# Performance work log

Hardware: AMD Instinct MI355X
Metric: run time of the kernel (lower is better)

The kernel has to match this reference:

```python
import jax, jax.numpy as jnp
import numpy as np

IN_DIM = 8192
OUT_DIM = 4096
NNZ = 1638400
BATCH = 4096


def setup_inputs() -> dict:
    key = jax.random.key(0)
    k_x, k_r, k_c, k_w = jax.random.split(key, 4)
    x = jax.random.normal(k_x, (BATCH, IN_DIM), dtype=jnp.float32)
    row_idx = jax.random.randint(k_r, (NNZ,), 0, IN_DIM, dtype=jnp.int64)
    col_idx = jax.random.randint(k_c, (NNZ,), 0, OUT_DIM, dtype=jnp.int64)
    # xavier_uniform on a [nnz, 1] tensor: bound = sqrt(6 / (nnz + 1))
    bound = float(np.sqrt(6.0 / (NNZ + 1)))
    weights = jax.random.uniform(k_w, (NNZ,), dtype=jnp.float32, minval=-bound, maxval=bound)
    bias = jnp.zeros((OUT_DIM,), dtype=jnp.float32)
    return {"x": x, "row_idx": row_idx, "col_idx": col_idx, "weights": weights, "bias": bias}


def reference(x, row_idx, col_idx, weights, bias):
    # scatter_nd: build dense [IN_DIM, OUT_DIM] weight matrix via scatter-add
    ind1d = row_idx * OUT_DIM + col_idx  # flat indices, duplicates accumulate
    W = jnp.zeros((IN_DIM * OUT_DIM,), dtype=weights.dtype).at[ind1d].add(weights)
    W = W.reshape(IN_DIM, OUT_DIM)
    # dense matmul + bias, matching torch.mm(x, sparse_tensor) + bias
    return x @ W + bias
```

## Files before the change

kernel.cpp:

```cpp
#include <hip/hip_runtime.h>
#include <stdint.h>

#define IN_DIM 8192
#define OUT_DIM 4096
#define NNZ 1638400
#define BATCH 4096

typedef __bf16 bf16x8 __attribute__((ext_vector_type(8)));
typedef float f32x4 __attribute__((ext_vector_type(4)));


__device__ __forceinline__ unsigned short f2bf(float f) {
  union { float f; unsigned int u; } v; v.f = f;
  unsigned int u = v.u;
  unsigned int r = (u + 0x7FFFu + ((u >> 16) & 1u)) >> 16;
  return (unsigned short)r;
}

__device__ __forceinline__ float bf2f(unsigned short b) {
  union { unsigned int u; float f; } v;
  v.u = (unsigned int)b << 16;
  return v.f;
}

__device__ __forceinline__ void async16(const void* g, void* l) {
  __builtin_amdgcn_global_load_lds(
      (const __attribute__((address_space(1))) unsigned int*)g,
      (__attribute__((address_space(3))) unsigned int*)l,
      16, 0, 0);
}

__device__ __forceinline__ void convert_body(int i, const float* __restrict__ src,
                                             unsigned short* __restrict__ dst) {
  const float4* s = (const float4*)src;
  float4 a = s[2 * i];
  float4 b = s[2 * i + 1];
  union { unsigned short us[8]; uint4 v; } o;
  o.us[0] = f2bf(a.x); o.us[1] = f2bf(a.y); o.us[2] = f2bf(a.z); o.us[3] = f2bf(a.w);
  o.us[4] = f2bf(b.x); o.us[5] = f2bf(b.y); o.us[6] = f2bf(b.z); o.us[7] = f2bf(b.w);
  ((uint4*)dst)[i] = o.v;
}


#define PREP_BLOCKS ((IN_DIM * OUT_DIM) / 8 / 256)

__global__ void prep_kernel(uint4* __restrict__ W_zero,
                            const float* __restrict__ x,
                            unsigned short* __restrict__ x_bf16) {
  int i = blockIdx.x * 256 + threadIdx.x;
  W_zero[i] = make_uint4(0, 0, 0, 0);
  convert_body(i, x, x_bf16);
}


__device__ __forceinline__ void scat1(int c, int r, float w,
                                      unsigned int* __restrict__ W) {
  size_t e = (size_t)c * IN_DIM + r;
  unsigned int* p = W + (e >> 1);
  const bool hi = (e & 1);
  unsigned int cur = *p;
  unsigned int assumed;
  do {
    assumed = cur;
    unsigned short h = hi ? (unsigned short)(assumed >> 16)
                          : (unsigned short)(assumed & 0xFFFFu);
    unsigned short nb = f2bf(bf2f(h) + w);
    unsigned int nw = hi ? ((assumed & 0x0000FFFFu) | ((unsigned int)nb << 16))
                         : ((assumed & 0xFFFF0000u) | (unsigned int)nb);
    cur = atomicCAS(p, assumed, nw);
  } while (cur != assumed);
}

#define SCAT_BLOCKS (NNZ / 4 / 256)

__global__ void scatter_kernel(const int4* __restrict__ ri4,
                               const int4* __restrict__ ci4,
                               const float4* __restrict__ w4,
                               unsigned int* __restrict__ W) {
  int i = blockIdx.x * 256 + threadIdx.x;
  int4 r = ri4[i];
  int4 c = ci4[i];
  float4 w = w4[i];
  scat1(c.x, r.x, w.x, W);
  scat1(c.y, r.y, w.y, W);
  scat1(c.z, r.z, w.z, W);
  scat1(c.w, r.w, w.w, W);
}


#define TBM 256
#define TBN 256
#define TBK 64
#define NKT (IN_DIM / TBK)

__global__ __launch_bounds__(512, 2) void gemm_kernel(
    const unsigned short* __restrict__ A,
    const unsigned short* __restrict__ Bt,
    const float* __restrict__ bias,
    float* __restrict__ C) {
  extern __shared__ __align__(16) unsigned short lds[];

  const int tid = threadIdx.x;

  const int bid = blockIdx.x;
  const int xcd = bid & 7;
  const int j = bid >> 3;
  const int m0 = ((xcd & 1) * 8 + (j & 7)) * TBM;
  const int n0 = ((xcd >> 1) * 4 + (j >> 3)) * TBN;

  const int wid = tid >> 6;
  const int lane = tid & 63;
  const int wm = wid >> 2;
  const int wn = wid & 3;
  const int quad = lane >> 4;
  const int lm = lane & 15;
  const int xorv = lm & 7;

  const unsigned short* Ab = A + (size_t)m0 * IN_DIM;
  const unsigned short* Bb = Bt + (size_t)n0 * IN_DIM;

  int soff[4], ldst[4];
#pragma unroll
  for (int c = 0; c < 4; ++c) {
    const int t2 = c * 512 + tid;
    const int srow = t2 >> 3;
    const int sgs = (t2 & 7) ^ (srow & 7);
    soff[c] = srow * IN_DIM + sgs * 8;
    ldst[c] = t2 * 16;
  }

  f32x4 acc[8][4] = {};

#define STAGE(kt_, b_, c_)                                                  \
  do {                                                                      \
    const int k0_ = (kt_)*TBK;                                              \
    char* la_ = (char*)lds + (b_)*65536;                                    \
    async16(Ab + (size_t)soff[c_] + k0_, la_ + ldst[c_]);                   \
    async16(Bb + (size_t)soff[c_] + k0_, la_ + 32768 + ldst[c_]);           \
  } while (0)

#pragma unroll
  for (int c = 0; c < 4; ++c) STAGE(0, 0, c);

  for (int kt = 0; kt < NKT; ++kt) {
    const int buf = kt & 1;
    const int nbuf = buf ^ 1;
    const int ktn = (kt + 1) & (NKT - 1);

    asm volatile("s_waitcnt vmcnt(0)" ::: "memory");
    __builtin_amdgcn_sched_barrier(0);
    __builtin_amdgcn_s_barrier();
    __builtin_amdgcn_sched_barrier(0);

#pragma unroll
    for (int c = 0; c < 4; ++c) STAGE(ktn, nbuf, c);

    const unsigned short* lA = lds + buf * 32768;
    const unsigned short* lB = lA + 16384;

    bf16x8 bfr[4][2];
#pragma unroll
    for (int j2 = 0; j2 < 4; ++j2) {
      const int row = wn * 64 + j2 * 16 + lm;
#pragma unroll
      for (int ss = 0; ss < 2; ++ss) {
        const int p = ((ss << 2) | quad) ^ xorv;
        bfr[j2][ss] = *(const bf16x8*)(lB + row * TBK + p * 8);
      }
    }

#pragma unroll
    for (int q = 0; q < 4; ++q) {
      bf16x8 af[2][2];
#pragma unroll
      for (int i = 0; i < 2; ++i) {
        const int row = wm * 128 + (q * 2 + i) * 16 + lm;
#pragma unroll
        for (int ss = 0; ss < 2; ++ss) {
          const int p = ((ss << 2) | quad) ^ xorv;
          af[i][ss] = *(const bf16x8*)(lA + row * TBK + p * 8);
        }
      }
      __builtin_amdgcn_s_setprio(1);
#pragma unroll
      for (int i = 0; i < 2; ++i)
#pragma unroll
        for (int j2 = 0; j2 < 4; ++j2)
#pragma unroll
          for (int ss = 0; ss < 2; ++ss)
            acc[q * 2 + i][j2] = __builtin_amdgcn_mfma_f32_16x16x32_bf16(
                af[i][ss], bfr[j2][ss], acc[q * 2 + i][j2], 0, 0, 0);
      __builtin_amdgcn_s_setprio(0);
    }
  }
#undef STAGE

  asm volatile("s_waitcnt vmcnt(0)" ::: "memory");

  const int ccol0 = n0 + wn * 64 + lm;
  const int crow0 = m0 + wm * 128;
#pragma unroll
  for (int j2 = 0; j2 < 4; ++j2) {
    const int col = ccol0 + j2 * 16;
    const float bv = bias[col];
#pragma unroll
    for (int i = 0; i < 8; ++i) {
#pragma unroll
      for (int v = 0; v < 4; ++v) {
        const int row = crow0 + i * 16 + quad * 4 + v;
        C[(size_t)row * OUT_DIM + col] = acc[i][j2][v] + bv;
      }
    }
  }
}


extern "C" void kernel_launch(void* const* d_in, const int* in_sizes, int n_in,
                              void* d_out, int out_size, void* d_ws, size_t ws_size,
                              hipStream_t stream) {
  const float* x = (const float*)d_in[0];
  const int* row_idx = (const int*)d_in[1];
  const int* col_idx = (const int*)d_in[2];
  const float* weights = (const float*)d_in[3];
  const float* bias = (const float*)d_in[4];
  float* out = (float*)d_out;

  const size_t W_BF16_BYTES = (size_t)IN_DIM * OUT_DIM * 2;
  unsigned short* W_bf16 = (unsigned short*)d_ws;
  unsigned short* x_bf16 = (unsigned short*)((char*)d_ws + W_BF16_BYTES);

  static bool attr_set = false;
  if (!attr_set) {
    (void)hipFuncSetAttribute((const void*)gemm_kernel,
                              hipFuncAttributeMaxDynamicSharedMemorySize,
                              131072);
    attr_set = true;
  }

  prep_kernel<<<PREP_BLOCKS, 256, 0, stream>>>((uint4*)W_bf16, x, x_bf16);

  scatter_kernel<<<SCAT_BLOCKS, 256, 0, stream>>>(
      (const int4*)row_idx, (const int4*)col_idx, (const float4*)weights,
      (unsigned int*)W_bf16);

  gemm_kernel<<<dim3(256), dim3(512), 131072, stream>>>(x_bf16, W_bf16, bias, out);
}
```

Measured before the change: 506.6 us.

## Software-pipeline LDS fragment reads across K-tiles in the GEMM main loop

Restructures the GEMM K loop, unrolled by two with ping-pong register sets, so the B fragments and first A fragments for the next tile are read from LDS before the last MFMA group of the current tile runs. The global-load wait and barrier move to inside the tile, so LDS read latency at the start of each tile overlaps with MFMA work. The cost is more live registers from the doubled fragment sets, which could cause spills under the 2-blocks-per-CU launch bound. It also adds a second barrier per tile.

```diff
diff --git a/kernel.cpp b/kernel.cpp
--- a/kernel.cpp
+++ b/kernel.cpp
@@ -104,9 +104,9 @@
 
   const int bid = blockIdx.x;
   const int xcd = bid & 7;
-  const int j = bid >> 3;
-  const int m0 = ((xcd & 1) * 8 + (j & 7)) * TBM;
-  const int n0 = ((xcd >> 1) * 4 + (j >> 3)) * TBN;
+  const int jb = bid >> 3;
+  const int m0 = ((xcd & 1) * 8 + (jb & 7)) * TBM;
+  const int n0 = ((xcd >> 1) * 4 + (jb >> 3)) * TBN;
 
   const int wid = tid >> 6;
   const int lane = tid & 63;
@@ -139,60 +139,95 @@
     async16(Bb + (size_t)soff[c_] + k0_, la_ + 32768 + ldst[c_]);           \
   } while (0)
 
+#define RD_AF(lAp_, q_, AFD)                                                \
+  do {                                                                      \
+    _Pragma("unroll") for (int i = 0; i < 2; ++i) {                         \
+      const int row = wm * 128 + ((q_)*2 + i) * 16 + lm;                    \
+      _Pragma("unroll") for (int ss = 0; ss < 2; ++ss) {                    \
+        const int p = ((ss << 2) | quad) ^ xorv;                            \
+        AFD[i][ss] = *(const bf16x8*)((lAp_) + row * TBK + p * 8);          \
+      }                                                                     \
+    }                                                                       \
+  } while (0)
+
+#define RD_BF(lBp_, BFD)                                                    \
+  do {                                                                      \
+    _Pragma("unroll") for (int j2 = 0; j2 < 4; ++j2) {                      \
+      const int row = wn * 64 + j2 * 16 + lm;                               \
+      _Pragma("unroll") for (int ss = 0; ss < 2; ++ss) {                    \
+        const int p = ((ss << 2) | quad) ^ xorv;                            \
+        BFD[j2][ss] = *(const bf16x8*)((lBp_) + row * TBK + p * 8);         \
+      }                                                                     \
+    }                                                                       \
+  } while (0)
+
+#define MFMA_Q(q_, AF, BFR)                                                 \
+  do {                                                                      \
+    __builtin_amdgcn_s_setprio(1);                                          \
+    _Pragma("unroll") for (int i = 0; i < 2; ++i)                           \
+    _Pragma("unroll") for (int j2 = 0; j2 < 4; ++j2)                        \
+    _Pragma("unroll") for (int ss = 0; ss < 2; ++ss)                        \
+      acc[(q_)*2 + i][j2] = __builtin_amdgcn_mfma_f32_16x16x32_bf16(        \
+          AF[i][ss], BFR[j2][ss], acc[(q_)*2 + i][j2], 0, 0, 0);            \
+    __builtin_amdgcn_s_setprio(0);                                          \
+  } while (0)
+
+#define TILE(t_, buf_, BFRC, AFC, BFRN, AFN)                                \
+  do {                                                                      \
+    const int nb_ = (buf_) ^ 1;                                             \
+    const int ktn_ = ((t_) + 1) & (NKT - 1);                                \
+    const unsigned short* lA_ = lds + (buf_)*32768;                         \
+                  \
+    __builtin_amdgcn_sched_barrier(0);                                      \
+    __builtin_amdgcn_s_barrier();                                           \
+    __builtin_amdgcn_sched_barrier(0);                                      \
+    _Pragma("unroll") for (int c = 0; c < 4; ++c) STAGE(ktn_, nb_, c);      \
+                                   \
+    MFMA_Q(0, AFC, BFRC);                                                   \
+    {                                                                       \
+      bf16x8 afx[2][2];                                                     \
+      RD_AF(lA_, 1, afx);                                                   \
+      MFMA_Q(1, afx, BFRC);                                                 \
+    }                                                                       \
+    {                                                                       \
+      bf16x8 afx[2][2];                                                     \
+      RD_AF(lA_, 2, afx);                                                   \
+      MFMA_Q(2, afx, BFRC);                                                 \
+    }                                                                       \
+    {                                                                       \
+      bf16x8 afx[2][2];                                                     \
+      RD_AF(lA_, 3, afx);                                                   \
+            \
+      asm volatile("s_waitcnt vmcnt(0)" ::: "memory");                      \
+      __builtin_amdgcn_sched_barrier(0);                                    \
+      __builtin_amdgcn_s_barrier();                                         \
+      __builtin_amdgcn_sched_barrier(0);                                    \
+                             \
+      RD_BF(lds + nb_*32768 + 16384, BFRN);                                 \
+      RD_AF(lds + nb_*32768, 0, AFN);                                       \
+      MFMA_Q(3, afx, BFRC);                                                 \
+    }                                                                       \
+  } while (0)
+
 #pragma unroll
   for (int c = 0; c < 4; ++c) STAGE(0, 0, c);
-
-  for (int kt = 0; kt < NKT; ++kt) {
-    const int buf = kt & 1;
-    const int nbuf = buf ^ 1;
-    const int ktn = (kt + 1) & (NKT - 1);
-
-    asm volatile("s_waitcnt vmcnt(0)" ::: "memory");
-    __builtin_amdgcn_sched_barrier(0);
-    __builtin_amdgcn_s_barrier();
-    __builtin_amdgcn_sched_barrier(0);
-
-#pragma unroll
-    for (int c = 0; c < 4; ++c) STAGE(ktn, nbuf, c);
-
-    const unsigned short* lA = lds + buf * 32768;
-    const unsigned short* lB = lA + 16384;
-
-    bf16x8 bfr[4][2];
-#pragma unroll
-    for (int j2 = 0; j2 < 4; ++j2) {
-      const int row = wn * 64 + j2 * 16 + lm;
-#pragma unroll
-      for (int ss = 0; ss < 2; ++ss) {
-        const int p = ((ss << 2) | quad) ^ xorv;
-        bfr[j2][ss] = *(const bf16x8*)(lB + row * TBK + p * 8);
-      }
-    }
-
-#pragma unroll
-    for (int q = 0; q < 4; ++q) {
-      bf16x8 af[2][2];
-#pragma unroll
-      for (int i = 0; i < 2; ++i) {
-        const int row = wm * 128 + (q * 2 + i) * 16 + lm;
-#pragma unroll
-        for (int ss = 0; ss < 2; ++ss) {
-          const int p = ((ss << 2) | quad) ^ xorv;
-          af[i][ss] = *(const bf16x8*)(lA + row * TBK + p * 8);
-        }
-      }
-      __builtin_amdgcn_s_setprio(1);
-#pragma unroll
-      for (int i = 0; i < 2; ++i)
-#pragma unroll
-        for (int j2 = 0; j2 < 4; ++j2)
-#pragma unroll
-          for (int ss = 0; ss < 2; ++ss)
-            acc[q * 2 + i][j2] = __builtin_amdgcn_mfma_f32_16x16x32_bf16(
-                af[i][ss], bfr[j2][ss], acc[q * 2 + i][j2], 0, 0, 0);
-      __builtin_amdgcn_s_setprio(0);
-    }
-  }
+  asm volatile("s_waitcnt vmcnt(0)" ::: "memory");
+  __builtin_amdgcn_sched_barrier(0);
+  __builtin_amdgcn_s_barrier();
+  __builtin_amdgcn_sched_barrier(0);
+  bf16x8 bfrP[4][2], bfrQ[4][2], afP[2][2], afQ[2][2];
+  RD_BF(lds + 16384, bfrP);
+  RD_AF(lds, 0, afP);
+
+  for (int kt = 0; kt < NKT; kt += 2) {
+    TILE(kt, 0, bfrP, afP, bfrQ, afQ);
+    TILE(kt + 1, 1, bfrQ, afQ, bfrP, afP);
+  }
+
+#undef TILE
+#undef MFMA_Q
+#undef RD_BF
+#undef RD_AF
 #undef STAGE
 
   asm volatile("s_waitcnt vmcnt(0)" ::: "memory");
```

Result: slower. 663.7 us (+31.0%).

## Replace async global-to-LDS loads with register-staged prefetch two tiles ahead

Applied to the files above, without the earlier changes.

The GEMM main loop stops using global_load_lds direct copies. It now loads the tile two iterations ahead into registers and writes the previous register-staged tile into the spare LDS buffer after the MFMA work, with one barrier per iteration. The aim is to hide global latency behind a full iteration of compute instead of waiting on vmcnt(0) at the top of each iteration. The cost is eight extra uint4 registers per thread and explicit ds_write instructions, which may pressure occupancy at launch_bounds(512,2). The COMMIT stores also have to wait on their global loads, which can stall.

```diff
diff --git a/kernel.cpp b/kernel.cpp
--- a/kernel.cpp
+++ b/kernel.cpp
@@ -21,13 +21,6 @@
   union { unsigned int u; float f; } v;
   v.u = (unsigned int)b << 16;
   return v.f;
-}
-
-__device__ __forceinline__ void async16(const void* g, void* l) {
-  __builtin_amdgcn_global_load_lds(
-      (const __attribute__((address_space(1))) unsigned int*)g,
-      (__attribute__((address_space(3))) unsigned int*)l,
-      16, 0, 0);
 }
 
 __device__ __forceinline__ void convert_body(int i, const float* __restrict__ src,
@@ -104,9 +97,9 @@
 
   const int bid = blockIdx.x;
   const int xcd = bid & 7;
-  const int j = bid >> 3;
-  const int m0 = ((xcd & 1) * 8 + (j & 7)) * TBM;
-  const int n0 = ((xcd >> 1) * 4 + (j >> 3)) * TBN;
+  const int jb = bid >> 3;
+  const int m0 = ((xcd & 1) * 8 + (jb & 7)) * TBM;
+  const int n0 = ((xcd >> 1) * 4 + (jb >> 3)) * TBN;
 
   const int wid = tid >> 6;
   const int lane = tid & 63;
@@ -131,29 +124,38 @@
 
   f32x4 acc[8][4] = {};
 
-#define STAGE(kt_, b_, c_)                                                  \
+  uint4 sA[4], sB[4];
+
+#define LOADG(kt_)                                                          \
   do {                                                                      \
     const int k0_ = (kt_)*TBK;                                              \
+    _Pragma("unroll") for (int c = 0; c < 4; ++c) {                         \
+      sA[c] = *(const uint4*)(Ab + (size_t)soff[c] + k0_);                  \
+      sB[c] = *(const uint4*)(Bb + (size_t)soff[c] + k0_);                  \
+    }                                                                       \
+  } while (0)
+
+#define COMMIT(b_)                                                          \
+  do {                                                                      \
     char* la_ = (char*)lds + (b_)*65536;                                    \
-    async16(Ab + (size_t)soff[c_] + k0_, la_ + ldst[c_]);                   \
-    async16(Bb + (size_t)soff[c_] + k0_, la_ + 32768 + ldst[c_]);           \
+    _Pragma("unroll") for (int c = 0; c < 4; ++c) {                         \
+      *(uint4*)(la_ + ldst[c]) = sA[c];                                     \
+      *(uint4*)(la_ + 32768 + ldst[c]) = sB[c];                             \
+    }                                                                       \
   } while (0)
 
-#pragma unroll
-  for (int c = 0; c < 4; ++c) STAGE(0, 0, c);
+  LOADG(0);
+  COMMIT(0);
+  LOADG(1);
+  asm volatile("s_waitcnt lgkmcnt(0)" ::: "memory");
+  __builtin_amdgcn_sched_barrier(0);
+  __builtin_amdgcn_s_barrier();
+  __builtin_amdgcn_sched_barrier(0);
 
   for (int kt = 0; kt < NKT; ++kt) {
     const int buf = kt & 1;
     const int nbuf = buf ^ 1;
-    const int ktn = (kt + 1) & (NKT - 1);
-
-    asm volatile("s_waitcnt vmcnt(0)" ::: "memory");
-    __builtin_amdgcn_sched_barrier(0);
-    __builtin_amdgcn_s_barrier();
-    __builtin_amdgcn_sched_barrier(0);
-
-#pragma unroll
-    for (int c = 0; c < 4; ++c) STAGE(ktn, nbuf, c);
+    const int kt2 = (kt + 2) & (NKT - 1);
 
     const unsigned short* lA = lds + buf * 32768;
     const unsigned short* lB = lA + 16384;
@@ -192,10 +194,16 @@
                 af[i][ss], bfr[j2][ss], acc[q * 2 + i][j2], 0, 0, 0);
       __builtin_amdgcn_s_setprio(0);
     }
-  }
-#undef STAGE
-
-  asm volatile("s_waitcnt vmcnt(0)" ::: "memory");
+
+    COMMIT(nbuf);
+    LOADG(kt2);
+    asm volatile("s_waitcnt lgkmcnt(0)" ::: "memory");
+    __builtin_amdgcn_sched_barrier(0);
+    __builtin_amdgcn_s_barrier();
+    __builtin_amdgcn_sched_barrier(0);
+  }
+#undef COMMIT
+#undef LOADG
 
   const int ccol0 = n0 + wn * 64 + lm;
   const int crow0 = m0 + wm * 128;
```

Result: slower. 1.048 ms (+106.8%).
